# Kernel tuning notes

Measured on AMD Instinct MI355X. Metric: run time of the kernel, lower is better.

The kernel has to match this reference:

```python
import jax, jax.numpy as jnp
import numpy as np

NUM_NODES = 15000


def _gcn_conv(x, W, b, src, dst, norm, num_nodes):
    # PyG GCNConv: x' = D^-1/2 (A + I) D^-1/2 (x W) + b
    h = x @ W                                   # [N, out]
    msg = h[src] * norm[:, None]                # gather + scale per edge
    out = jax.ops.segment_sum(msg, dst, num_segments=num_nodes)
    return out + b


def setup_inputs() -> dict:
    key = jax.random.key(0)
    ks = jax.random.split(key, 12)
    T = 100000
    E = 200000
    inp = {
        "x": jax.random.normal(ks[0], (NUM_NODES, 768), jnp.float32),
        "r_emb": jax.random.normal(ks[1], (T, 768), jnp.float32),
        "W1": jax.random.normal(ks[2], (768, 10), jnp.float32) * 0.05,
        "b1": jax.random.normal(ks[3], (10,), jnp.float32) * 0.05,
        "W2": jax.random.normal(ks[4], (10, 128), jnp.float32) * 0.05,
        "b2": jax.random.normal(ks[5], (128,), jnp.float32) * 0.05,
        "W_ih": jax.random.normal(ks[6], (512, 1024), jnp.float32) * 0.03,
        "W_hh": jax.random.normal(ks[7], (512, 128), jnp.float32) * 0.03,
        "b_ih": jax.random.normal(ks[8], (512,), jnp.float32) * 0.03,
        "b_hh": jax.random.normal(ks[9], (512,), jnp.float32) * 0.03,
        "edge_index": jax.random.randint(ks[10], (2, E), 0, NUM_NODES).astype(jnp.int64),
        "triples": jax.random.randint(ks[11], (T, 3), 0, NUM_NODES).astype(jnp.int64),
    }
    return inp


def reference(x, r_emb, W1, b1, W2, b2, W_ih, W_hh, b_ih, b_hh, edge_index, triples):
    N = x.shape[0]
    H = 128  # lstm hidden size
    # --- add self loops, symmetric GCN normalization ---
    loop = jnp.arange(N, dtype=edge_index.dtype)
    src = jnp.concatenate([edge_index[0], loop])
    dst = jnp.concatenate([edge_index[1], loop])
    deg = jax.ops.segment_sum(jnp.ones_like(dst, jnp.float32), dst, num_segments=N)
    dinv = jnp.where(deg > 0, jax.lax.rsqrt(deg), 0.0)
    norm = dinv[src] * dinv[dst]                      # [E+N]
    # --- 2-layer GCN ---
    h = jax.nn.relu(_gcn_conv(x, W1, b1, src, dst, norm, N))   # [N, 10]
    z = _gcn_conv(h, W2, b2, src, dst, norm, N)                # [N, 128]
    # --- per-triple LSTM scoring, batched (seq_len=1, zero init state) ---
    hvec = z[triples[:, 0]]                           # [T, 128]
    tvec = z[triples[:, 2]]                           # [T, 128]
    feat = jnp.concatenate([hvec, r_emb, tvec], axis=-1)       # [T, 1024]
    gates = feat @ W_ih.T + (b_ih + b_hh)             # [T, 512]; h0=0 so W_hh term vanishes
    i_g, f_g, g_g, o_g = jnp.split(gates, 4, axis=-1)  # torch gate order i,f,g,o
    c = jax.nn.sigmoid(i_g) * jnp.tanh(g_g)           # c0 = 0 -> forget term drops
    out = jax.nn.sigmoid(o_g) * jnp.tanh(c)           # [T, 128]
    score = jax.nn.sigmoid(jnp.sum(out, axis=-1))     # [T]
    return score
```

## Files before the change

kernel.cpp:

```cpp
#include <hip/hip_runtime.h>

#define NF 768
#define D1 10
#define D2 128
#define BM 64

typedef __attribute__((ext_vector_type(8))) short bf16x8;
typedef __attribute__((ext_vector_type(16))) float f32x16;

static __device__ __forceinline__ float sigf(float v){ return 1.0f/(1.0f+__expf(-v)); }
static __device__ __forceinline__ float tanhfast(float v){ return 2.0f/(1.0f+__expf(-2.0f*v)) - 1.0f; }
static __device__ __forceinline__ short f2bf(float f){
    unsigned u = __float_as_uint(f);
    u += 0x7fffu + ((u>>16)&1u);
    return (short)(u>>16);
}

static __device__ __forceinline__ void gload16(const void* g, void* l){
    __builtin_amdgcn_global_load_lds(
        (const __attribute__((address_space(1))) unsigned int*)(unsigned long long)g,
        (__attribute__((address_space(3))) unsigned int*)(unsigned long long)l,
        16, 0, 0);
}

static __device__ __forceinline__ bf16x8 cvt8(float4 a, float4 b){
    unsigned u0,u1,u2,u3;
    asm("v_cvt_pk_bf16_f32 %0, %1, %2" : "=v"(u0) : "v"(a.x), "v"(a.y));
    asm("v_cvt_pk_bf16_f32 %0, %1, %2" : "=v"(u1) : "v"(a.z), "v"(a.w));
    asm("v_cvt_pk_bf16_f32 %0, %1, %2" : "=v"(u2) : "v"(b.x), "v"(b.y));
    asm("v_cvt_pk_bf16_f32 %0, %1, %2" : "=v"(u3) : "v"(b.z), "v"(b.w));
    union { unsigned u[4]; bf16x8 v; } r;
    r.u[0]=u0; r.u[1]=u1; r.u[2]=u2; r.u[3]=u3;
    return r.v;
}

__global__ void k_deg(const int* __restrict__ dst, int* __restrict__ cnt, int E){
    int e = blockIdx.x*256 + threadIdx.x;
    if(e<E) atomicAdd(&cnt[dst[e]], 1);
}

__global__ __launch_bounds__(256) void k_scan(const int* __restrict__ cnt,
                                              int* __restrict__ rowptr, int* __restrict__ rowcur,
                                              float* __restrict__ dinv, int N, int E){
    __shared__ int part[256];
    int t = threadIdx.x;
    int C = (N+255)/256;
    int lo = t*C, hi = lo+C; if(hi>N) hi=N; if(lo>N) lo=N;
    int s=0;
    for(int i=lo;i<hi;i++) s += cnt[i];
    part[t]=s;
    __syncthreads();
    if(t==0){
        int run=0;
        for(int i=0;i<256;i++){ int v=part[i]; part[i]=run; run+=v; }
        rowptr[N]=E;
    }
    __syncthreads();
    int run = part[t];
    for(int i=lo;i<hi;i++){
        rowptr[i]=run; rowcur[i]=run; run += cnt[i];
        dinv[i] = rsqrtf((float)cnt[i] + 1.0f);
    }
}

__global__ void k_fill(const int* __restrict__ src, const int* __restrict__ dst,
                       const float* __restrict__ dinv, int* __restrict__ rowcur,
                       int* __restrict__ esrc, float* __restrict__ enorm, int E){
    int e = blockIdx.x*256 + threadIdx.x;
    if(e>=E) return;
    int s=src[e], d=dst[e];
    int pos = atomicAdd(&rowcur[d], 1);
    esrc[pos]=s;
    enorm[pos]=dinv[s]*dinv[d];
}

__global__ __launch_bounds__(256) void k_h1(const float* __restrict__ x,
                                            const float* __restrict__ W1,
                                            float* __restrict__ h1, int N){
    __shared__ float wt[D1*NF];
    for(int idx=threadIdx.x; idx<NF*D1; idx+=256){
        int k=idx/D1, c=idx-k*D1;
        wt[c*NF+k]=W1[idx];
    }
    __syncthreads();
    int row = blockIdx.x*4 + (threadIdx.x>>6);
    int lane = threadIdx.x&63;
    if(row>=N) return;
    const float4* xr = (const float4*)(x + (size_t)row*NF);
    float acc[D1];
#pragma unroll
    for(int c=0;c<D1;c++) acc[c]=0.f;
#pragma unroll
    for(int i=0;i<3;i++){
        float4 v = xr[lane + 64*i];
#pragma unroll
        for(int c=0;c<D1;c++){
            float4 w = *(const float4*)&wt[c*NF + (lane+64*i)*4];
            acc[c] += v.x*w.x + v.y*w.y + v.z*w.z + v.w*w.w;
        }
    }
#pragma unroll
    for(int c=0;c<D1;c++){
        float v=acc[c];
#pragma unroll
        for(int off=32;off;off>>=1) v += __shfl_down(v,off,64);
        acc[c]=v;
    }
    if(lane==0){
#pragma unroll
        for(int c=0;c<D1;c++) h1[(size_t)row*D1+c]=acc[c];
    }
}

__global__ __launch_bounds__(256) void k_gath1(const float* __restrict__ h1,
        const int* __restrict__ rowptr, const int* __restrict__ esrc,
        const float* __restrict__ enorm, const float* __restrict__ dinv,
        const float* __restrict__ b1, float* __restrict__ h, int N){
    int node = blockIdx.x*4 + (threadIdx.x>>6);
    int lane = threadIdx.x&63;
    if(node>=N) return;
    int e0=rowptr[node], e1=rowptr[node+1];
    float acc[D1];
#pragma unroll
    for(int c=0;c<D1;c++) acc[c]=0.f;
    for(int e=e0+lane; e<e1; e+=64){
        int s=esrc[e]; float w=enorm[e];
        const float* hr = h1 + (size_t)s*D1;
#pragma unroll
        for(int c=0;c<D1;c++) acc[c] += hr[c]*w;
    }
    if(lane==0){
        float di=dinv[node], d2=di*di;
        const float* hr = h1 + (size_t)node*D1;
#pragma unroll
        for(int c=0;c<D1;c++) acc[c] += hr[c]*d2;
    }
#pragma unroll
    for(int c=0;c<D1;c++){
        float v=acc[c];
#pragma unroll
        for(int off=32;off;off>>=1) v += __shfl_down(v,off,64);
        acc[c]=v;
    }
    if(lane==0){
#pragma unroll
        for(int c=0;c<D1;c++){
            float v = acc[c] + b1[c];
            h[(size_t)node*D1+c] = v>0.f ? v : 0.f;
        }
    }
}

__global__ __launch_bounds__(128) void k_hz(const float* __restrict__ h,
                                            const float* __restrict__ W2,
                                            float* __restrict__ hz, int N){
    __shared__ float w2s[D1*D2];
    int j = threadIdx.x;
    for(int i=j;i<D1*D2;i+=128) w2s[i]=W2[i];
    __syncthreads();
    int n = blockIdx.x;
    if(n>=N) return;
    const float* hr = h + (size_t)n*D1;
    float acc=0.f;
#pragma unroll
    for(int k=0;k<D1;k++) acc += hr[k]*w2s[k*D2+j];
    hz[(size_t)n*D2+j]=acc;
}

__global__ __launch_bounds__(128) void k_gath2(const float* __restrict__ hz,
        const int* __restrict__ rowptr, const int* __restrict__ esrc,
        const float* __restrict__ enorm, const float* __restrict__ dinv,
        const float* __restrict__ b2, float* __restrict__ zbf, int N){
    int n = blockIdx.x;
    int c = threadIdx.x;
    int e0 = rowptr[n], e1 = rowptr[n+1];
    float di = dinv[n];
    float acc = hz[(size_t)n*D2+c]*di*di + b2[c];
    int e = e0;
    for(; e+1<e1; e+=2){
        int s0=esrc[e], s1=esrc[e+1];
        float w0=enorm[e], w1=enorm[e+1];
        acc += hz[(size_t)s0*D2+c]*w0 + hz[(size_t)s1*D2+c]*w1;
    }
    if(e<e1) acc += hz[(size_t)esrc[e]*D2+c]*enorm[e];
    zbf[(size_t)n*D2+c] = acc;
}

__global__ void k_wimgB(const float* __restrict__ Wih, ushort* __restrict__ img){
    int gid = blockIdx.x*256 + threadIdx.x;
    if(gid >= 12*64*64) return;
    int l = gid & 63;
    int ks16 = (gid>>6) & 63;
    int f = gid >> 12;
    int dd = l & 31, kb = l>>5;
    int wn = f/3, gi = f - wn*3;
    int gbase = (gi==0)?0:((gi==1)?256:384);
    int wrow = gbase + wn*32 + dd;
    int k = ks16*16 + kb*8;
    const float* p = Wih + (size_t)wrow*1024 + k;
    float4 v0=*(const float4*)p, v1=*(const float4*)(p+4);
    bf16x8 o;
    o[0]=f2bf(v0.x); o[1]=f2bf(v0.y); o[2]=f2bf(v0.z); o[3]=f2bf(v0.w);
    o[4]=f2bf(v1.x); o[5]=f2bf(v1.y); o[6]=f2bf(v1.z); o[7]=f2bf(v1.w);
    *(bf16x8*)(img + (size_t)gid*8) = o;
}

__global__ __launch_bounds__(256,2) void k_big(
    const float* __restrict__ remb, const ushort* __restrict__ img,
    const float* __restrict__ zbf, const float* __restrict__ b_ih,
    const float* __restrict__ b_hh, const int* __restrict__ trip,
    float* __restrict__ score, int T)
{
    __shared__ float ring[4][64*64];
    int tid=threadIdx.x, lane=tid&63, w=tid>>6;
    int l31=lane&31, lh=lane>>5;
    int t0=blockIdx.x*BM;

    const int l16 = lane>>4;
    size_t rbo[4]; const float* zh4[4]; const float* zt4[4]; int lsl[4];
#pragma unroll
    for(int j=0;j<4;j++){
        int row = w*16 + j*4 + l16;
        int tc = t0 + row; if(tc>=T) tc=T-1;
        rbo[j] = (size_t)tc*NF;
        int th = trip[3*tc], tt = trip[3*tc+2];
        zh4[j] = zbf + (size_t)th*D2;
        zt4[j] = zbf + (size_t)tt*D2;
        lsl[j] = ((lane&15) ^ (row&15))*4;
    }

    const ushort* wb0 = img + ((size_t)(w*3+0)*64*64 + lane)*8;
    const ushort* wb1 = img + ((size_t)(w*3+1)*64*64 + lane)*8;
    const ushort* wb2 = img + ((size_t)(w*3+2)*64*64 + lane)*8;
    const int base0 = l31*64;
    const int base1 = (32+l31)*64;
    const int rx = lane&15;

    f32x16 acc[2][3];
    const f32x16 zer = {0,0,0,0,0,0,0,0,0,0,0,0,0,0,0,0};
#pragma unroll
    for(int m=0;m<2;m++)
#pragma unroll
        for(int g=0;g<3;g++) acc[m][g]=zer;

#define ISSUE(C_) { \
    float* dst_ = &ring[(C_)&3][(w*16)*64]; \
    _Pragma("unroll") \
    for(int j_=0;j_<4;j_++){ \
        const float* src_; \
        if((C_)<2)       src_ = zh4[j_] + (C_)*64 + lsl[j_]; \
        else if((C_)<14) src_ = remb + rbo[j_] + ((C_)-2)*64 + lsl[j_]; \
        else             src_ = zt4[j_] + ((C_)-14)*64 + lsl[j_]; \
        gload16(src_, dst_ + j_*4*64); \
    } }

    ISSUE(0) ISSUE(1) ISSUE(2)
    bf16x8 qb[2][3];
    qb[0][0]=*(const bf16x8*)(wb0);     qb[0][1]=*(const bf16x8*)(wb1);     qb[0][2]=*(const bf16x8*)(wb2);
    qb[1][0]=*(const bf16x8*)(wb0+512); qb[1][1]=*(const bf16x8*)(wb1+512); qb[1][2]=*(const bf16x8*)(wb2+512);

#define KSTEP(C_,S_) { \
    const float4 a00_ = *(const float4*)&cur_[base0 + ((((S_)*4+lh*2)  )^rx)*4]; \
    const float4 a01_ = *(const float4*)&cur_[base0 + ((((S_)*4+lh*2)+1)^rx)*4]; \
    const float4 a10_ = *(const float4*)&cur_[base1 + ((((S_)*4+lh*2)  )^rx)*4]; \
    const float4 a11_ = *(const float4*)&cur_[base1 + ((((S_)*4+lh*2)+1)^rx)*4]; \
    bf16x8 A0_ = cvt8(a00_, a01_); \
    bf16x8 A1_ = cvt8(a10_, a11_); \
    bf16x8 B0_=qb[(S_)&1][0], B1_=qb[(S_)&1][1], B2_=qb[(S_)&1][2]; \
    if((C_)*4+(S_)+2 < 64){ \
        size_t ko_ = (size_t)((C_)*4+(S_)+2)*512; \
        qb[(S_)&1][0]=*(const bf16x8*)(wb0+ko_); \
        qb[(S_)&1][1]=*(const bf16x8*)(wb1+ko_); \
        qb[(S_)&1][2]=*(const bf16x8*)(wb2+ko_); \
    } \
    acc[0][0]=__builtin_amdgcn_mfma_f32_32x32x16_bf16(A0_,B0_,acc[0][0],0,0,0); \
    acc[0][1]=__builtin_amdgcn_mfma_f32_32x32x16_bf16(A0_,B1_,acc[0][1],0,0,0); \
    acc[0][2]=__builtin_amdgcn_mfma_f32_32x32x16_bf16(A0_,B2_,acc[0][2],0,0,0); \
    acc[1][0]=__builtin_amdgcn_mfma_f32_32x32x16_bf16(A1_,B0_,acc[1][0],0,0,0); \
    acc[1][1]=__builtin_amdgcn_mfma_f32_32x32x16_bf16(A1_,B1_,acc[1][1],0,0,0); \
    acc[1][2]=__builtin_amdgcn_mfma_f32_32x32x16_bf16(A1_,B2_,acc[1][2],0,0,0); \
}

#define CHUNK(C_) { \
    asm volatile("s_waitcnt vmcnt(12)" ::: "memory"); \
    __builtin_amdgcn_s_barrier(); \
    __builtin_amdgcn_sched_barrier(0); \
    if((C_)+3 < 16) { ISSUE((C_)+3) } \
    const float* cur_ = &ring[(C_)&3][0]; \
    __builtin_amdgcn_s_setprio(1); \
    KSTEP(C_,0) KSTEP(C_,1) KSTEP(C_,2) KSTEP(C_,3) \
    __builtin_amdgcn_s_setprio(0); \
}

    CHUNK(0)  CHUNK(1)  CHUNK(2)  CHUNK(3)
    CHUNK(4)  CHUNK(5)  CHUNK(6)  CHUNK(7)
    CHUNK(8)  CHUNK(9)  CHUNK(10) CHUNK(11)
    CHUNK(12) CHUNK(13) CHUNK(14) CHUNK(15)
#undef CHUNK
#undef KSTEP
#undef ISSUE

    float* rowsum = &ring[0][0];
    __syncthreads();
    if(tid<BM) rowsum[tid]=0.f;
    __syncthreads();
    int d = w*32+l31;
    float bi=b_ih[d]+b_hh[d];
    float bg=b_ih[256+d]+b_hh[256+d];
    float bo=b_ih[384+d]+b_hh[384+d];
#pragma unroll
    for(int m=0;m<2;m++){
#pragma unroll
        for(int r=0;r<16;r++){
            int row = m*32 + (r&3)+8*(r>>2)+4*lh;
            float ig = acc[m][0][r] + bi;
            float gg = acc[m][1][r] + bg;
            float og = acc[m][2][r] + bo;
            float cc = sigf(ig)*tanhfast(gg);
            float ov = sigf(og)*tanhfast(cc);
#pragma unroll
            for(int off=1; off<32; off<<=1) ov += __shfl_xor(ov, off, 64);
            if(l31==0) atomicAdd(&rowsum[row], ov);
        }
    }
    __syncthreads();
    if(tid < BM){
        int t = t0 + tid;
        if(t < T) score[t] = sigf(rowsum[tid]);
    }
}

extern "C" void kernel_launch(void* const* d_in, const int* in_sizes, int n_in,
                              void* d_out, int out_size, void* d_ws, size_t ws_size,
                              hipStream_t stream){
    const float* x    = (const float*)d_in[0];
    const float* remb = (const float*)d_in[1];
    const float* W1   = (const float*)d_in[2];
    const float* b1   = (const float*)d_in[3];
    const float* W2   = (const float*)d_in[4];
    const float* b2   = (const float*)d_in[5];
    const float* Wih  = (const float*)d_in[6];
    const float* b_ih = (const float*)d_in[8];
    const float* b_hh = (const float*)d_in[9];
    const int*   ei   = (const int*)d_in[10];
    const int*   trip = (const int*)d_in[11];
    float* score = (float*)d_out;

    const int N = in_sizes[0]/NF;
    const int E = in_sizes[10]/2;
    const int T = in_sizes[11]/3;
    const int* src = ei;
    const int* dst = ei + E;

    float* ws = (float*)d_ws;
    size_t o = 0;
    ushort* img  = (ushort*)(ws+o); o += (size_t)12*64*64*8/2;
    float* zbf   = ws+o;            o += (size_t)N*D2;
    int*   cnt    = (int*)(ws+o);   o += (size_t)((N+8)&~7);
    int*   rowptr = (int*)(ws+o);   o += (size_t)((N+8)&~7);
    int*   rowcur = (int*)(ws+o);   o += (size_t)((N+8)&~7);
    int*   esrc   = (int*)(ws+o);   o += (size_t)E;
    float* enorm  = ws+o;           o += (size_t)E;
    float* dinv   = ws+o;           o += (size_t)((N+7)&~7);
    float* h1     = ws+o;           o += (size_t)N*D1;
    float* hbuf   = ws+o;           o += (size_t)N*D1;
    float* hz     = ws+o;           o += (size_t)N*D2;
    (void)ws_size; (void)n_in; (void)out_size;

    hipMemsetAsync(cnt, 0, (size_t)N*sizeof(int), stream);

    k_wimgB<<<dim3((12*64*64+255)/256), dim3(256), 0, stream>>>(Wih, img);
    k_deg  <<<dim3((E+255)/256), dim3(256), 0, stream>>>(dst, cnt, E);
    k_scan <<<dim3(1), dim3(256), 0, stream>>>(cnt, rowptr, rowcur, dinv, N, E);
    k_fill <<<dim3((E+255)/256), dim3(256), 0, stream>>>(src, dst, dinv, rowcur, esrc, enorm, E);
    k_h1   <<<dim3((N+3)/4), dim3(256), 0, stream>>>(x, W1, h1, N);
    k_gath1<<<dim3((N+3)/4), dim3(256), 0, stream>>>(h1, rowptr, esrc, enorm, dinv, b1, hbuf, N);
    k_hz   <<<dim3(N), dim3(128), 0, stream>>>(hbuf, W2, hz, N);
    k_gath2<<<dim3(N), dim3(128), 0, stream>>>(hz, rowptr, esrc, enorm, dinv, b2, zbf, N);
    k_big  <<<dim3((T+BM-1)/BM), dim3(256), 0, stream>>>(remb, img, zbf, b_ih, b_hh, trip, score, T);
}
```

Measured before the change: 316.3 us.

## Prefetch weight fragments a full chunk ahead with per-chunk vmcnt waits

Replaces the per-k-step two-deep register prefetch of W_ih bf16 fragments with a whole-chunk double buffer (12 fragments per chunk) issued right after each barrier. The vmcnt wait counts are retuned per chunk so that they cover both the LDS async loads and the weight loads, and sched_barriers pin the issue order. Pointer precomputation is replaced by integer indices to save registers. The goal is to hide weight-fetch latency behind MFMA work. The cost is much higher VGPR pressure under launch_bounds(256,2), which may spill or reduce occupancy.

```diff
diff --git a/kernel.cpp b/kernel.cpp
--- a/kernel.cpp
+++ b/kernel.cpp
@@ -217,15 +217,14 @@
     int t0=blockIdx.x*BM;
 
     const int l16 = lane>>4;
-    size_t rbo[4]; const float* zh4[4]; const float* zt4[4]; int lsl[4];
+    int tc4[4], th4[4], tt4[4], lsl[4];
 #pragma unroll
     for(int j=0;j<4;j++){
         int row = w*16 + j*4 + l16;
         int tc = t0 + row; if(tc>=T) tc=T-1;
-        rbo[j] = (size_t)tc*NF;
-        int th = trip[3*tc], tt = trip[3*tc+2];
-        zh4[j] = zbf + (size_t)th*D2;
-        zt4[j] = zbf + (size_t)tt*D2;
+        tc4[j] = tc;
+        th4[j] = trip[3*tc];
+        tt4[j] = trip[3*tc+2];
         lsl[j] = ((lane&15) ^ (row&15))*4;
     }
 
@@ -243,62 +242,69 @@
 #pragma unroll
         for(int g=0;g<3;g++) acc[m][g]=zer;
 
+    bf16x8 qb[2][4][3];
+
+#define BISSUE(CN_) if((CN_)<16){ \
+    _Pragma("unroll") \
+    for(int s_=0;s_<4;s_++){ \
+        size_t ko_ = (size_t)((CN_)*4+s_)*512; \
+        qb[(CN_)&1][s_][0] = *(const bf16x8*)(wb0+ko_); \
+        qb[(CN_)&1][s_][1] = *(const bf16x8*)(wb1+ko_); \
+        qb[(CN_)&1][s_][2] = *(const bf16x8*)(wb2+ko_); \
+    } }
+
 #define ISSUE(C_) { \
     float* dst_ = &ring[(C_)&3][(w*16)*64]; \
     _Pragma("unroll") \
     for(int j_=0;j_<4;j_++){ \
         const float* src_; \
-        if((C_)<2)       src_ = zh4[j_] + (C_)*64 + lsl[j_]; \
-        else if((C_)<14) src_ = remb + rbo[j_] + ((C_)-2)*64 + lsl[j_]; \
-        else             src_ = zt4[j_] + ((C_)-14)*64 + lsl[j_]; \
-        gload16(src_, dst_ + j_*4*64); \
+        if((C_)<2)       src_ = zbf + (size_t)th4[j_]*D2 + (C_)*64 + lsl[j_]; \
+        else if((C_)<14) src_ = remb + (size_t)tc4[j_]*NF + ((C_)-2)*64 + lsl[j_]; \
+        else             src_ = zbf + (size_t)tt4[j_]*D2 + ((C_)-14)*64 + lsl[j_]; \
+        gload16(src_, dst_ + j_*256); \
     } }
-
-    ISSUE(0) ISSUE(1) ISSUE(2)
-    bf16x8 qb[2][3];
-    qb[0][0]=*(const bf16x8*)(wb0);     qb[0][1]=*(const bf16x8*)(wb1);     qb[0][2]=*(const bf16x8*)(wb2);
-    qb[1][0]=*(const bf16x8*)(wb0+512); qb[1][1]=*(const bf16x8*)(wb1+512); qb[1][2]=*(const bf16x8*)(wb2+512);
 
 #define KSTEP(C_,S_) { \
     const float4 a00_ = *(const float4*)&cur_[base0 + ((((S_)*4+lh*2)  )^rx)*4]; \
     const float4 a01_ = *(const float4*)&cur_[base0 + ((((S_)*4+lh*2)+1)^rx)*4]; \
+    bf16x8 A0_ = cvt8(a00_, a01_); \
     const float4 a10_ = *(const float4*)&cur_[base1 + ((((S_)*4+lh*2)  )^rx)*4]; \
     const float4 a11_ = *(const float4*)&cur_[base1 + ((((S_)*4+lh*2)+1)^rx)*4]; \
-    bf16x8 A0_ = cvt8(a00_, a01_); \
     bf16x8 A1_ = cvt8(a10_, a11_); \
-    bf16x8 B0_=qb[(S_)&1][0], B1_=qb[(S_)&1][1], B2_=qb[(S_)&1][2]; \
-    if((C_)*4+(S_)+2 < 64){ \
-        size_t ko_ = (size_t)((C_)*4+(S_)+2)*512; \
-        qb[(S_)&1][0]=*(const bf16x8*)(wb0+ko_); \
-        qb[(S_)&1][1]=*(const bf16x8*)(wb1+ko_); \
-        qb[(S_)&1][2]=*(const bf16x8*)(wb2+ko_); \
-    } \
-    acc[0][0]=__builtin_amdgcn_mfma_f32_32x32x16_bf16(A0_,B0_,acc[0][0],0,0,0); \
-    acc[0][1]=__builtin_amdgcn_mfma_f32_32x32x16_bf16(A0_,B1_,acc[0][1],0,0,0); \
-    acc[0][2]=__builtin_amdgcn_mfma_f32_32x32x16_bf16(A0_,B2_,acc[0][2],0,0,0); \
-    acc[1][0]=__builtin_amdgcn_mfma_f32_32x32x16_bf16(A1_,B0_,acc[1][0],0,0,0); \
-    acc[1][1]=__builtin_amdgcn_mfma_f32_32x32x16_bf16(A1_,B1_,acc[1][1],0,0,0); \
-    acc[1][2]=__builtin_amdgcn_mfma_f32_32x32x16_bf16(A1_,B2_,acc[1][2],0,0,0); \
-}
-
-#define CHUNK(C_) { \
-    asm volatile("s_waitcnt vmcnt(12)" ::: "memory"); \
+    acc[0][0]=__builtin_amdgcn_mfma_f32_32x32x16_bf16(A0_,qb[(C_)&1][S_][0],acc[0][0],0,0,0); \
+    acc[0][1]=__builtin_amdgcn_mfma_f32_32x32x16_bf16(A0_,qb[(C_)&1][S_][1],acc[0][1],0,0,0); \
+    acc[0][2]=__builtin_amdgcn_mfma_f32_32x32x16_bf16(A0_,qb[(C_)&1][S_][2],acc[0][2],0,0,0); \
+    acc[1][0]=__builtin_amdgcn_mfma_f32_32x32x16_bf16(A1_,qb[(C_)&1][S_][0],acc[1][0],0,0,0); \
+    acc[1][1]=__builtin_amdgcn_mfma_f32_32x32x16_bf16(A1_,qb[(C_)&1][S_][1],acc[1][1],0,0,0); \
+    acc[1][2]=__builtin_amdgcn_mfma_f32_32x32x16_bf16(A1_,qb[(C_)&1][S_][2],acc[1][2],0,0,0); \
+}
+
+#define CHUNK(C_,W_) { \
+    asm volatile("s_waitcnt vmcnt(" W_ ")" ::: "memory"); \
+    __builtin_amdgcn_sched_barrier(0); \
     __builtin_amdgcn_s_barrier(); \
+    BISSUE((C_)+1) \
     __builtin_amdgcn_sched_barrier(0); \
     if((C_)+3 < 16) { ISSUE((C_)+3) } \
+    __builtin_amdgcn_sched_barrier(0); \
     const float* cur_ = &ring[(C_)&3][0]; \
     __builtin_amdgcn_s_setprio(1); \
     KSTEP(C_,0) KSTEP(C_,1) KSTEP(C_,2) KSTEP(C_,3) \
     __builtin_amdgcn_s_setprio(0); \
 }
 
-    CHUNK(0)  CHUNK(1)  CHUNK(2)  CHUNK(3)
-    CHUNK(4)  CHUNK(5)  CHUNK(6)  CHUNK(7)
-    CHUNK(8)  CHUNK(9)  CHUNK(10) CHUNK(11)
-    CHUNK(12) CHUNK(13) CHUNK(14) CHUNK(15)
+    BISSUE(0)
+    __builtin_amdgcn_sched_barrier(0);
+    ISSUE(0) ISSUE(1) ISSUE(2)
+
+    CHUNK(0 ,"8")  CHUNK(1 ,"20") CHUNK(2 ,"32") CHUNK(3 ,"32")
+    CHUNK(4 ,"32") CHUNK(5 ,"32") CHUNK(6 ,"32") CHUNK(7 ,"32")
+    CHUNK(8 ,"32") CHUNK(9 ,"32") CHUNK(10,"32") CHUNK(11,"32")
+    CHUNK(12,"32") CHUNK(13,"32") CHUNK(14,"28") CHUNK(15,"24")
 #undef CHUNK
 #undef KSTEP
 #undef ISSUE
+#undef BISSUE
 
     float* rowsum = &ring[0][0];
     __syncthreads();
```

Measured after the change: 316.6 us. No clear change (+0.1%).
